# Performance work log

Measured on AMD Instinct MI355X. Metric: run time of the kernel, lower is better.

The kernel has to match this reference:

```python
import jax, jax.numpy as jnp
import numpy as np
import math

C_IN, L, D, H, DFF = 16, 1024, 128, 8, 512
B = 16
EPS = 1e-5


def layer_norm(x, g, b):
    mu = jnp.mean(x, axis=-1, keepdims=True)
    var = jnp.var(x, axis=-1, keepdims=True)
    return (x - mu) * jax.lax.rsqrt(var + EPS) * g + b


def tape_pe():
    pos = jnp.arange(L, dtype=jnp.float32)[:, None]
    div = jnp.exp(jnp.arange(0, D, 2, dtype=jnp.float32) * (-math.log(10000.0) / D))
    ang = pos * div * (D / L)  # [L, D/2]
    return jnp.stack([jnp.sin(ang), jnp.cos(ang)], axis=-1).reshape(L, D)


def setup_inputs() -> dict:
    key = jax.random.key(0)
    ks = jax.random.split(key, 16)
    d4 = 4 * D
    inp = {
        "x": jax.random.normal(ks[0], (B, C_IN, L), dtype=jnp.float32),
        "conv1_w": jax.random.normal(ks[1], (d4, 1, 1, 7), dtype=jnp.float32) * 0.2,
        "conv1_b": jnp.zeros((d4,), jnp.float32),
        "bn1_g": jnp.ones((d4,), jnp.float32),
        "bn1_b": jnp.zeros((d4,), jnp.float32),
        "conv2_w": jax.random.normal(ks[2], (D, d4, C_IN, 1), dtype=jnp.float32) * (1.0 / math.sqrt(d4 * C_IN)),
        "conv2_b": jnp.zeros((D,), jnp.float32),
        "bn2_g": jnp.ones((D,), jnp.float32),
        "bn2_b": jnp.zeros((D,), jnp.float32),
        "wq": jax.random.normal(ks[3], (D, D), dtype=jnp.float32) / math.sqrt(D),
        "wk": jax.random.normal(ks[4], (D, D), dtype=jnp.float32) / math.sqrt(D),
        "wv": jax.random.normal(ks[5], (D, D), dtype=jnp.float32) / math.sqrt(D),
        "rel_table": jax.random.normal(ks[6], (2 * L - 1, H), dtype=jnp.float32) * 0.02,
        "ln_att_g": jnp.ones((D,), jnp.float32),
        "ln_att_b": jnp.zeros((D,), jnp.float32),
        "ln1_g": jnp.ones((D,), jnp.float32),
        "ln1_b": jnp.zeros((D,), jnp.float32),
        "ln2_g": jnp.ones((D,), jnp.float32),
        "ln2_b": jnp.zeros((D,), jnp.float32),
        "ff_w1": jax.random.normal(ks[7], (DFF, D), dtype=jnp.float32) / math.sqrt(D),
        "ff_b1": jnp.zeros((DFF,), jnp.float32),
        "ff_w2": jax.random.normal(ks[8], (D, DFF), dtype=jnp.float32) / math.sqrt(DFF),
        "ff_b2": jnp.zeros((D,), jnp.float32),
    }
    return inp


def reference(x, conv1_w, conv1_b, bn1_g, bn1_b, conv2_w, conv2_b, bn2_g, bn2_b,
              wq, wk, wv, rel_table, ln_att_g, ln_att_b, ln1_g, ln1_b,
              ln2_g, ln2_b, ff_w1, ff_b1, ff_w2, ff_b2):
    dn = ("NCHW", "OIHW", "NCHW")
    h = x[:, None, :, :]  # [B,1,C_IN,L]
    h = jax.lax.conv_general_dilated(h, conv1_w, (1, 1), ((0, 0), (3, 3)), dimension_numbers=dn)
    h = h + conv1_b[None, :, None, None]
    # BatchNorm2d in eval with running_mean=0, running_var=1
    h = h * (bn1_g * (1.0 / math.sqrt(1.0 + EPS)))[None, :, None, None] + bn1_b[None, :, None, None]
    h = jax.nn.gelu(h, approximate=False)
    h = jax.lax.conv_general_dilated(h, conv2_w, (1, 1), ((0, 0), (0, 0)), dimension_numbers=dn)
    h = h + conv2_b[None, :, None, None]
    h = h * (bn2_g * (1.0 / math.sqrt(1.0 + EPS)))[None, :, None, None] + bn2_b[None, :, None, None]
    h = jax.nn.gelu(h, approximate=False)
    x_src = jnp.transpose(h[:, :, 0, :], (0, 2, 1))  # [B,L,D]

    x_pos = x_src + tape_pe()  # tAPE (dropout is identity in eval)

    dh = D // H
    scale = D ** (-0.5)  # note: full d_model, as in the source
    q = (x_pos @ wq.T).reshape(B, L, H, dh).transpose(0, 2, 1, 3)
    k = (x_pos @ wk.T).reshape(B, L, H, dh).transpose(0, 2, 1, 3)
    v = (x_pos @ wv.T).reshape(B, L, H, dh).transpose(0, 2, 1, 3)
    scores = jnp.einsum("bhqd,bhkd->bhqk", q, k) * scale
    attn = jax.nn.softmax(scores, axis=-1)
    # gathered relative-position bias added AFTER softmax (faithful to source)
    idx = jnp.arange(L)[:, None] - jnp.arange(L)[None, :] + (L - 1)  # [L,L]
    rel_bias = rel_table[idx]  # [L,L,H]
    attn = attn + jnp.transpose(rel_bias, (2, 0, 1))[None]
    out = jnp.einsum("bhqk,bhkd->bhqd", attn, v).transpose(0, 2, 1, 3).reshape(B, L, D)
    out = layer_norm(out, ln_att_g, ln_att_b)  # Attention_Rel_Scl.to_out

    att = layer_norm(x_src + out, ln1_g, ln1_b)
    ff = jax.nn.relu(att @ ff_w1.T + ff_b1) @ ff_w2.T + ff_b2
    y = layer_norm(att + ff, ln2_g, ln2_b)
    return jnp.transpose(y, (0, 2, 1))  # [B,D,L]
```

## Files before the change

### kernel.cpp

```cpp
#include <hip/hip_runtime.h>
#include <math.h>

#define BB   16
#define CIN  16
#define LL   1024
#define DD   128
#define NHH  8
#define DHH  16
#define DF   512

#define INVS 0.9999950000374998f
#define QSCALE2 0.12751743f

typedef __attribute__((ext_vector_type(4))) float f32x4;
typedef __attribute__((ext_vector_type(8))) __bf16 bf16x8;

__device__ __forceinline__ float gelu_t(float v) {
    float u = v * v;
    float a = v * fmaf(-0.07135481627f, u, -1.5957691216f);
    float e = __expf(a);
    return v * __builtin_amdgcn_rcpf(1.0f + e);
}

__device__ __forceinline__ unsigned pkbf(float a, float b) {
    union { __bf16 h[2]; unsigned u; } z;
    z.h[0] = (__bf16)a; z.h[1] = (__bf16)b;
    return z.u;
}

#define SWZ(l) ((((l) & 7) ^ (((l) >> 2) & 6)))

__global__ __launch_bounds__(256) void k_prep(
    const float* __restrict__ c2w,
    const float* __restrict__ wq, const float* __restrict__ wk,
    const float* __restrict__ wv,
    const float* __restrict__ w1f, const float* __restrict__ w2f,
    const float* __restrict__ c1w, const float* __restrict__ c1b,
    const float* __restrict__ g1,  const float* __restrict__ bb1,
    __bf16* __restrict__ w2bf,  __bf16* __restrict__ wallbf,
    __bf16* __restrict__ w1fbf, __bf16* __restrict__ w2fbf,
    float* __restrict__ peb, float* __restrict__ w1A, float* __restrict__ b1A)
{
    const int bid = blockIdx.x;
    const int t = threadIdx.x;
    if (bid < 1024) {
        int i = (bid * 256 + t) * 4;
        float4 v = *(const float4*)&c2w[i];
        union { __bf16 h[4]; float2 f2; } u;
        u.h[0] = (__bf16)v.x; u.h[1] = (__bf16)v.y;
        u.h[2] = (__bf16)v.z; u.h[3] = (__bf16)v.w;
        *(float2*)&w2bf[i] = u.f2;
    } else if (bid < 1072) {
        int e = ((bid - 1024) * 256 + t) * 4;
        int sel = e >> 14, r = e & 16383;
        const float* src = (sel == 0) ? wq : ((sel == 1) ? wk : wv);
        float sc = (sel == 0) ? QSCALE2 : 1.0f;
        float4 v = *(const float4*)&src[r];
        union { __bf16 h[4]; float2 f2; } u;
        u.h[0] = (__bf16)(v.x * sc); u.h[1] = (__bf16)(v.y * sc);
        u.h[2] = (__bf16)(v.z * sc); u.h[3] = (__bf16)(v.w * sc);
        *(float2*)&wallbf[e] = u.f2;
    } else if (bid < 1136) {
        int e = ((bid - 1072) * 256 + t) * 4;
        float4 v = *(const float4*)&w1f[e];
        union { __bf16 h[4]; float2 f2; } u;
        u.h[0] = (__bf16)v.x; u.h[1] = (__bf16)v.y;
        u.h[2] = (__bf16)v.z; u.h[3] = (__bf16)v.w;
        *(float2*)&w1fbf[e] = u.f2;
    } else if (bid < 1200) {
        int e = ((bid - 1136) * 256 + t) * 4;
        float4 v = *(const float4*)&w2f[e];
        union { __bf16 h[4]; float2 f2; } u;
        u.h[0] = (__bf16)v.x; u.h[1] = (__bf16)v.y;
        u.h[2] = (__bf16)v.z; u.h[3] = (__bf16)v.w;
        *(float2*)&w2fbf[e] = u.f2;
    } else if (bid < 1456) {
        int p = (bid - 1200) * 256 + t;
        int l = p >> 6, jj = p & 63;
        float ang = (float)l * expf(-0.14391156831212787f * (float)jj) * 0.125f;
        peb[l * 128 + jj * 2]     = sinf(ang);
        peb[l * 128 + jj * 2 + 1] = cosf(ang);
    } else {
        for (int o = t; o < DF; o += 256) {
            float A = g1[o] * INVS;
            #pragma unroll
            for (int tp = 0; tp < 7; tp++) w1A[o * 8 + tp] = c1w[o * 7 + tp] * A;
            w1A[o * 8 + 7] = 0.0f;
            b1A[o] = fmaf(c1b[o], A, bb1[o]);
        }
    }
}

__global__ __launch_bounds__(512, 4) void k_conv(
    const float* __restrict__ x,
    const float* __restrict__ w1A, const float* __restrict__ b1A,
    const __bf16* __restrict__ w2bf,
    const float* __restrict__ c2b, const float* __restrict__ g2,
    const float* __restrict__ bb2,
    float* __restrict__ xsrc)
{
    const int lt = blockIdx.x;
    const int b  = blockIdx.y;
    const int t  = threadIdx.x;
    const int l0 = lt * 32;

    __shared__ float xs[CIN][40];
    __shared__ __align__(16) __bf16 Ab[2][32 * 256];

    for (int idx = t; idx < CIN * 38; idx += 512) {
        int c = idx / 38, i = idx % 38;
        int l = l0 - 3 + i;
        xs[c][i] = (l >= 0 && l < LL) ? x[(b * CIN + c) * LL + l] : 0.0f;
    }
    __syncthreads();

    const int lane = t & 63;
    const int wv   = t >> 6;
    const int ogu  = __builtin_amdgcn_readfirstlane(wv);
    const int cp   = lane & 7;
    const int lqi  = lane >> 3;
    const int c0   = cp * 2;
    const int lq   = lqi * 4;

    float xw[2][10];
    #pragma unroll
    for (int j = 0; j < 10; j++) {
        xw[0][j] = xs[c0][lq + j];
        xw[1][j] = xs[c0 + 1][lq + j];
    }

    const int l15 = lane & 15, kg = lane >> 4;

    f32x4 acc[2];
    acc[0] = (f32x4){0.f, 0.f, 0.f, 0.f};
    acc[1] = (f32x4){0.f, 0.f, 0.f, 0.f};

    bf16x8 breg[8];

#define BLOAD(CH) do { \
    _Pragma("unroll") \
    for (int kk = 0; kk < 8; kk++) \
        breg[kk] = *(const bf16x8*)&w2bf[ \
            (size_t)(wv * 16 + l15) * 8192 + (size_t)(CH) * 256 + kk * 32 + kg * 8]; \
} while (0)

#define CONV_CHUNK(BUF, CH) do { \
    _Pragma("unroll") \
    for (int j = 0; j < 2; j++) { \
        int o = (CH) * 16 + ogu * 2 + j; \
        f32x4 wA = *(const f32x4*)&w1A[o * 8]; \
        f32x4 wB = *(const f32x4*)&w1A[o * 8 + 4]; \
        float bias = b1A[o]; \
        int kcol = (ogu * 2 + j) * 16 + c0; \
        _Pragma("unroll") \
        for (int dl = 0; dl < 4; dl++) { \
            float h2[2]; \
            _Pragma("unroll") \
            for (int ci = 0; ci < 2; ci++) { \
                float s = fmaf(xw[ci][dl], wA[0], bias); \
                s = fmaf(xw[ci][dl + 1], wA[1], s); \
                s = fmaf(xw[ci][dl + 2], wA[2], s); \
                s = fmaf(xw[ci][dl + 3], wA[3], s); \
                s = fmaf(xw[ci][dl + 4], wB[0], s); \
                s = fmaf(xw[ci][dl + 5], wB[1], s); \
                s = fmaf(xw[ci][dl + 6], wB[2], s); \
                h2[ci] = gelu_t(s); \
            } \
            int l = lq + dl; \
            *(unsigned*)&Ab[BUF][l * 256 + (kcol ^ (SWZ(l) << 3))] = pkbf(h2[0], h2[1]); \
        } \
    } \
} while (0)

#define MFMA_CHUNK(BUF) do { \
    _Pragma("unroll") \
    for (int kk = 0; kk < 8; kk++) { \
        int kb = kk * 32 + kg * 8; \
        _Pragma("unroll") \
        for (int mf = 0; mf < 2; mf++) { \
            int r = mf * 16 + l15; \
            bf16x8 af = *(const bf16x8*)&Ab[BUF][r * 256 + (kb ^ (SWZ(r) << 3))]; \
            acc[mf] = __builtin_amdgcn_mfma_f32_16x16x32_bf16(af, breg[kk], acc[mf], 0, 0, 0); \
        } \
    } \
} while (0)

    BLOAD(0);
    CONV_CHUNK(0, 0);
    __syncthreads();

    for (int ic = 0; ic < 30; ic += 2) {
        MFMA_CHUNK(0);
        BLOAD(ic + 1);
        CONV_CHUNK(1, ic + 1);
        __syncthreads();

        MFMA_CHUNK(1);
        BLOAD(ic + 2);
        CONV_CHUNK(0, ic + 2);
        __syncthreads();
    }
    MFMA_CHUNK(0);
    BLOAD(31);
    CONV_CHUNK(1, 31);
    __syncthreads();
    MFMA_CHUNK(1);

    {
        int d = wv * 16 + l15;
        float A2 = g2[d] * INVS;
        float B2 = fmaf(c2b[d], A2, bb2[d]);
        #pragma unroll
        for (int mf = 0; mf < 2; mf++) {
            #pragma unroll
            for (int r = 0; r < 4; r++) {
                int l = l0 + mf * 16 + kg * 4 + r;
                xsrc[((size_t)b * LL + l) * DD + d] = gelu_t(fmaf(acc[mf][r], A2, B2));
            }
        }
    }
#undef BLOAD
#undef CONV_CHUNK
#undef MFMA_CHUNK
}

__global__ __launch_bounds__(384) void k_qkv(
    const float* __restrict__ xsrc, const float* __restrict__ peb,
    const __bf16* __restrict__ wallbf,
    __bf16* __restrict__ qo, __bf16* __restrict__ ko, __bf16* __restrict__ vo)
{
    const int lt = blockIdx.x, b = blockIdx.y;
    const int t = threadIdx.x;
    const int l0 = lt * 64;

    __shared__ __align__(16) __bf16 Xp[64 * 128];

    for (int e = t; e < 2048; e += 384) {
        int l = e >> 5, d0 = (e & 31) * 4;
        float4 xv = *(const float4*)&xsrc[((size_t)b * LL + l0 + l) * DD + d0];
        float4 pv = *(const float4*)&peb[(size_t)(l0 + l) * DD + d0];
        union { __bf16 h[4]; float2 f2; } u;
        u.h[0] = (__bf16)(xv.x + pv.x); u.h[1] = (__bf16)(xv.y + pv.y);
        u.h[2] = (__bf16)(xv.z + pv.z); u.h[3] = (__bf16)(xv.w + pv.w);
        *(float2*)&Xp[l * 128 + (d0 ^ (SWZ(l) << 3))] = u.f2;
    }
    __syncthreads();

    const int w = t >> 6, lane = t & 63;
    const int l15 = lane & 15, kg = lane >> 4;
    const int wsel = w >> 1, hb = w & 1;

    bf16x8 breg[16];
    #pragma unroll
    for (int nf = 0; nf < 4; nf++)
        #pragma unroll
        for (int kk = 0; kk < 4; kk++)
            breg[nf * 4 + kk] = *(const bf16x8*)&wallbf[
                (size_t)wsel * 16384 + (size_t)(hb * 64 + nf * 16 + l15) * 128 + kk * 32 + kg * 8];

    f32x4 acc[4][4];
    #pragma unroll
    for (int mf = 0; mf < 4; mf++)
        #pragma unroll
        for (int nf = 0; nf < 4; nf++) acc[mf][nf] = (f32x4){0.f, 0.f, 0.f, 0.f};

    #pragma unroll
    for (int kk = 0; kk < 4; kk++) {
        int kb = kk * 32 + kg * 8;
        bf16x8 af[4];
        #pragma unroll
        for (int mf = 0; mf < 4; mf++) {
            int r = mf * 16 + l15;
            af[mf] = *(const bf16x8*)&Xp[r * 128 + (kb ^ (SWZ(r) << 3))];
        }
        #pragma unroll
        for (int mf = 0; mf < 4; mf++)
            #pragma unroll
            for (int nf = 0; nf < 4; nf++)
                acc[mf][nf] = __builtin_amdgcn_mfma_f32_16x16x32_bf16(
                    af[mf], breg[nf * 4 + kk], acc[mf][nf], 0, 0, 0);
    }

    __bf16* op = (wsel == 0) ? qo : ((wsel == 1) ? ko : vo);
    #pragma unroll
    for (int mf = 0; mf < 4; mf++) {
        #pragma unroll
        for (int nf = 0; nf < 4; nf++) {
            int h = hb * 4 + nf;
            #pragma unroll
            for (int r = 0; r < 4; r++) {
                int l = l0 + mf * 16 + kg * 4 + r;
                op[(((size_t)b * NHH + h) * LL + l) * DHH + l15] = (__bf16)acc[mf][nf][r];
            }
        }
    }
}

__global__ __launch_bounds__(256) void k_attn(
    const __bf16* __restrict__ q, const __bf16* __restrict__ k,
    const __bf16* __restrict__ v, const float* __restrict__ rel,
    float* __restrict__ out)
{
    const int bh = blockIdx.x;
    const int qt = blockIdx.y;
    const int h  = bh & 7;
    const int t  = threadIdx.x;
    const int w  = t >> 6, lane = t & 63;
    const int g  = lane >> 4, qi = lane & 15;
    const int xq = (qi & 7) << 3;
    const int qbase = qt * 128 + w * 32;

    __shared__ __align__(16) __bf16 lds[16384];
    __bf16* Vl = lds;
    __bf16* Pw = lds + 4096 + w * 2048;
    __bf16* R0 = lds + 12288;
    __bf16* R1 = lds + 14336;

    for (int i = t; i < 2048; i += 256) {
        R0[i] = (__bf16)((i <= 2046) ? rel[(size_t)(2046 - i) * NHH + h] : 0.0f);
        R1[i] = (__bf16)((i <= 2045) ? rel[(size_t)(2045 - i) * NHH + h] : 0.0f);
    }

    bf16x8 qf[2];
    {
        union { unsigned u[4]; bf16x8 v8; } uz;
        uz.u[0] = uz.u[1] = uz.u[2] = uz.u[3] = 0u;
        #pragma unroll
        for (int n = 0; n < 2; n++) {
            qf[n] = uz.v8;
            if (g < 2)
                qf[n] = *(const bf16x8*)&q[((size_t)bh * LL + qbase + n * 16 + qi) * DHH + g * 8];
        }
    }

    f32x4 accp[2], accb[2];
    #pragma unroll
    for (int n = 0; n < 2; n++) {
        accp[n] = (f32x4){0.f, 0.f, 0.f, 0.f};
        accb[n] = (f32x4){0.f, 0.f, 0.f, 0.f};
    }
    float mrun[2] = {-INFINITY, -INFINITY};
    float lrun[2] = {0.f, 0.f};

    const f32x4 zero4 = (f32x4){0.f, 0.f, 0.f, 0.f};

#define PROC_N(Sn, n) do { \
    float mx = Sn[0][0]; \
    _Pragma("unroll") \
    for (int f = 0; f < 8; f++) { \
        _Pragma("unroll") \
        for (int r = 0; r < 4; r++) if (f || r) mx = fmaxf(mx, Sn[f][r]); } \
    mx = fmaxf(mx, __shfl_xor(mx, 16, 64)); \
    mx = fmaxf(mx, __shfl_xor(mx, 32, 64)); \
    float mnew = fmaxf(mrun[n], mx); \
    float sf = __builtin_amdgcn_exp2f(mrun[n] - mnew); \
    mrun[n] = mnew; \
    lrun[n] *= sf; \
    accp[n][0] *= sf; accp[n][1] *= sf; accp[n][2] *= sf; accp[n][3] *= sf; \
    float ls = 0.f; \
    _Pragma("unroll") \
    for (int f = 0; f < 8; f++) { \
        float p0 = __builtin_amdgcn_exp2f(Sn[f][0] - mnew); \
        float p1 = __builtin_amdgcn_exp2f(Sn[f][1] - mnew); \
        float p2 = __builtin_amdgcn_exp2f(Sn[f][2] - mnew); \
        float p3 = __builtin_amdgcn_exp2f(Sn[f][3] - mnew); \
        ls += (p0 + p1) + (p2 + p3); \
        unsigned* pp = (unsigned*)(Pw + (qi * 128 + ((f * 16 + g * 4) ^ xq))); \
        pp[0] = pkbf(p0, p1); pp[1] = pkbf(p2, p3); \
    } \
    ls += __shfl_xor(ls, 16, 64); ls += __shfl_xor(ls, 32, 64); \
    lrun[n] += ls; \
    int qoff = 1023 - (qbase + (n) * 16 + qi) + k0; \
    _Pragma("unroll") \
    for (int c = 0; c < 4; c++) { \
        bf16x8 vf = *(const bf16x8*)&Vbuf[qi * 128 + ((c * 32 + g * 8) ^ xq)]; \
        bf16x8 pf = *(const bf16x8*)&Pw[qi * 128 + ((c * 32 + g * 8) ^ xq)]; \
        int idx = qoff + c * 32 + 8 * g; \
        const unsigned* tb = (const unsigned*)((idx & 1) ? R1 : R0); \
        unsigned s_ = (unsigned)idx >> 1; \
        union { unsigned u[4]; bf16x8 v8; } bu; \
        bu.u[0] = tb[s_]; bu.u[1] = tb[s_ + 1]; \
        bu.u[2] = tb[s_ + 2]; bu.u[3] = tb[s_ + 3]; \
        accp[n] = __builtin_amdgcn_mfma_f32_16x16x32_bf16(vf, pf, accp[n], 0, 0, 0); \
        accb[n] = __builtin_amdgcn_mfma_f32_16x16x32_bf16(vf, bu.v8, accb[n], 0, 0, 0); \
    } \
} while (0)

    for (int kt = 0; kt < 8; kt++) {
        const int k0 = kt * 128;
        {
            int kr = t >> 1, d0 = (t & 1) * 8;
            bf16x8 b8 = *(const bf16x8*)&v[((size_t)bh * LL + k0 + kr) * DHH + d0];
            __bf16* dst = Vl + (kt & 1) * 2048;
            #pragma unroll
            for (int i = 0; i < 8; i++) {
                int d = d0 + i;
                dst[d * 128 + (kr ^ ((d & 7) << 3))] = b8[i];
            }
        }
        __syncthreads();
        const __bf16* Vbuf = Vl + (kt & 1) * 2048;

        f32x4 S0[8], S1[8];
        #pragma unroll
        for (int f = 0; f < 8; f++) {
            bf16x8 kf = *(const bf16x8*)&k[((size_t)bh * LL + k0 + f * 16 + qi) * DHH + (g & 1) * 8];
            S0[f] = __builtin_amdgcn_mfma_f32_16x16x32_bf16(kf, qf[0], zero4, 0, 0, 0);
            S1[f] = __builtin_amdgcn_mfma_f32_16x16x32_bf16(kf, qf[1], zero4, 0, 0, 0);
        }

        PROC_N(S0, 0);
        PROC_N(S1, 1);
    }
#undef PROC_N

    #pragma unroll
    for (int n = 0; n < 2; n++) {
        float inv = 1.0f / lrun[n];
        float4 o;
        o.x = accp[n][0] * inv + accb[n][0];
        o.y = accp[n][1] * inv + accb[n][1];
        o.z = accp[n][2] * inv + accb[n][2];
        o.w = accp[n][3] * inv + accb[n][3];
        *(float4*)&out[((size_t)bh * LL + qbase + n * 16 + qi) * DHH + g * 4] = o;
    }
}

__global__ __launch_bounds__(256) void k_ln(
    const float* __restrict__ ao,  const float* __restrict__ xsrc,
    const float* __restrict__ lag, const float* __restrict__ lab,
    const float* __restrict__ l1g, const float* __restrict__ l1b,
    float* __restrict__ att)
{
    const int lt = blockIdx.x, b = blockIdx.y;
    const int t = threadIdx.x;
    const int l0 = lt * 64;
    __shared__ float tile[64][132];

    #pragma unroll
    for (int u = 0; u < 4; u++) {
        int cid = u * 256 + t;
        int hh = cid >> 7, rem = cid & 127;
        int l = rem >> 1, dh0 = (rem & 1) * 8;
        const float* src = &ao[(((size_t)b * NHH + hh) * LL + l0 + l) * DHH + dh0];
        float4 a0 = *(const float4*)src;
        float4 a1 = *(const float4*)(src + 4);
        *(float4*)&tile[l][hh * 16 + dh0]     = a0;
        *(float4*)&tile[l][hh * 16 + dh0 + 4] = a1;
    }
    __syncthreads();

    const int wid = t >> 6, lane = t & 63;
    float2 ga  = *(const float2*)&lag[lane * 2];
    float2 ba  = *(const float2*)&lab[lane * 2];
    float2 g1v = *(const float2*)&l1g[lane * 2];
    float2 b1v = *(const float2*)&l1b[lane * 2];

    for (int rr = 0; rr < 16; rr++) {
        int r = wid * 16 + rr;
        float2 vv = *(const float2*)&tile[r][lane * 2];
        float s = vv.x + vv.y, s2 = vv.x * vv.x + vv.y * vv.y;
        #pragma unroll
        for (int m = 1; m < 64; m <<= 1) { s += __shfl_xor(s, m, 64); s2 += __shfl_xor(s2, m, 64); }
        float mu = s * (1.f / 128.f);
        float var = s2 * (1.f / 128.f) - mu * mu;
        float rs = rsqrtf(var + 1e-5f);
        float o0 = (vv.x - mu) * rs * ga.x + ba.x;
        float o1 = (vv.y - mu) * rs * ga.y + ba.y;
        float2 xv = *(const float2*)&xsrc[((size_t)b * LL + l0 + r) * DD + lane * 2];
        float t0 = xv.x + o0, t1 = xv.y + o1;
        s = t0 + t1; s2 = t0 * t0 + t1 * t1;
        #pragma unroll
        for (int m = 1; m < 64; m <<= 1) { s += __shfl_xor(s, m, 64); s2 += __shfl_xor(s2, m, 64); }
        mu = s * (1.f / 128.f);
        var = s2 * (1.f / 128.f) - mu * mu;
        rs = rsqrtf(var + 1e-5f);
        float a0 = (t0 - mu) * rs * g1v.x + b1v.x;
        float a1 = (t1 - mu) * rs * g1v.y + b1v.y;
        float2 o = {a0, a1};
        *(float2*)&att[((size_t)b * LL + l0 + r) * DD + lane * 2] = o;
    }
}

__global__ __launch_bounds__(512) void k_ff1(
    const float* __restrict__ att, const __bf16* __restrict__ w1fbf,
    const float* __restrict__ b1f, __bf16* __restrict__ ff1b)
{
    const int lt = blockIdx.x, b = blockIdx.y;
    const int t = threadIdx.x;
    const int l0 = lt * 64;

    __shared__ __align__(16) __bf16 Ax[64 * 128];

    #pragma unroll
    for (int it = 0; it < 4; it++) {
        int e = it * 512 + t;
        int l = e >> 5, d0 = (e & 31) * 4;
        float4 xv = *(const float4*)&att[((size_t)b * LL + l0 + l) * DD + d0];
        union { __bf16 h[4]; float2 f2; } u;
        u.h[0] = (__bf16)xv.x; u.h[1] = (__bf16)xv.y;
        u.h[2] = (__bf16)xv.z; u.h[3] = (__bf16)xv.w;
        *(float2*)&Ax[l * 128 + (d0 ^ (SWZ(l) << 3))] = u.f2;
    }
    __syncthreads();

    const int w = t >> 6, lane = t & 63;
    const int l15 = lane & 15, kg = lane >> 4;

    bf16x8 breg[16];
    #pragma unroll
    for (int nf = 0; nf < 4; nf++)
        #pragma unroll
        for (int kk = 0; kk < 4; kk++)
            breg[nf * 4 + kk] = *(const bf16x8*)&w1fbf[
                (size_t)(w * 64 + nf * 16 + l15) * 128 + kk * 32 + kg * 8];

    f32x4 acc[4][4];
    #pragma unroll
    for (int mf = 0; mf < 4; mf++)
        #pragma unroll
        for (int nf = 0; nf < 4; nf++) acc[mf][nf] = (f32x4){0.f, 0.f, 0.f, 0.f};

    #pragma unroll
    for (int kk = 0; kk < 4; kk++) {
        int kb = kk * 32 + kg * 8;
        bf16x8 af[4];
        #pragma unroll
        for (int mf = 0; mf < 4; mf++) {
            int r = mf * 16 + l15;
            af[mf] = *(const bf16x8*)&Ax[r * 128 + (kb ^ (SWZ(r) << 3))];
        }
        #pragma unroll
        for (int mf = 0; mf < 4; mf++)
            #pragma unroll
            for (int nf = 0; nf < 4; nf++)
                acc[mf][nf] = __builtin_amdgcn_mfma_f32_16x16x32_bf16(
                    af[mf], breg[nf * 4 + kk], acc[mf][nf], 0, 0, 0);
    }

    #pragma unroll
    for (int nf = 0; nf < 4; nf++) {
        int n = w * 64 + nf * 16 + l15;
        float bias = b1f[n];
        #pragma unroll
        for (int mf = 0; mf < 4; mf++) {
            #pragma unroll
            for (int r = 0; r < 4; r++) {
                int l = l0 + mf * 16 + kg * 4 + r;
                float vv = fmaxf(acc[mf][nf][r] + bias, 0.0f);
                ff1b[((size_t)b * LL + l) * DF + n] = (__bf16)vv;
            }
        }
    }
}

__global__ __launch_bounds__(512) void k_ff2(
    const __bf16* __restrict__ ff1b, const __bf16* __restrict__ w2fbf,
    const float* __restrict__ b2f, const float* __restrict__ att,
    const float* __restrict__ l2g, const float* __restrict__ l2b,
    float* __restrict__ y)
{
    const int lt = blockIdx.x, b = blockIdx.y;
    const int t = threadIdx.x;
    const int l0 = lt * 64;

    __shared__ __align__(16) __bf16 Ax[64 * 512];
    float* yl = (float*)Ax;

    #pragma unroll
    for (int it = 0; it < 8; it++) {
        int g8 = it * 512 + t;
        int l = g8 >> 6, c8 = g8 & 63;
        bf16x8 v8 = *(const bf16x8*)&ff1b[((size_t)b * LL + l0 + l) * DF + c8 * 8];
        *(bf16x8*)&Ax[l * 512 + ((c8 * 8) ^ (SWZ(l) << 3))] = v8;
    }
    __syncthreads();

    const int w = t >> 6, lane = t & 63;
    const int l15 = lane & 15, kg = lane >> 4;
    const int d = w * 16 + l15;

    bf16x8 breg[16];
    #pragma unroll
    for (int kk = 0; kk < 16; kk++)
        breg[kk] = *(const bf16x8*)&w2fbf[(size_t)d * DF + kk * 32 + kg * 8];

    f32x4 acc[4];
    #pragma unroll
    for (int mf = 0; mf < 4; mf++) acc[mf] = (f32x4){0.f, 0.f, 0.f, 0.f};

    #pragma unroll
    for (int kk = 0; kk < 16; kk++) {
        int kb = kk * 32 + kg * 8;
        #pragma unroll
        for (int mf = 0; mf < 4; mf++) {
            int r = mf * 16 + l15;
            bf16x8 af = *(const bf16x8*)&Ax[r * 512 + (kb ^ (SWZ(r) << 3))];
            acc[mf] = __builtin_amdgcn_mfma_f32_16x16x32_bf16(af, breg[kk], acc[mf], 0, 0, 0);
        }
    }
    __syncthreads();

    {
        float bias = b2f[d];
        #pragma unroll
        for (int mf = 0; mf < 4; mf++) {
            #pragma unroll
            for (int r = 0; r < 4; r++) {
                int l = mf * 16 + kg * 4 + r;
                float res = att[((size_t)b * LL + l0 + l) * DD + d];
                yl[l * 132 + d] = acc[mf][r] + bias + res;
            }
        }
    }
    __syncthreads();

    const int wid = t >> 6;
    float2 gv = *(const float2*)&l2g[lane * 2];
    float2 bv = *(const float2*)&l2b[lane * 2];
    for (int rr = 0; rr < 8; rr++) {
        int r = wid * 8 + rr;
        float2 vv = *(const float2*)&yl[r * 132 + lane * 2];
        float s = vv.x + vv.y, s2 = vv.x * vv.x + vv.y * vv.y;
        #pragma unroll
        for (int m = 1; m < 64; m <<= 1) { s += __shfl_xor(s, m, 64); s2 += __shfl_xor(s2, m, 64); }
        float mu = s * (1.f / 128.f);
        float var = s2 * (1.f / 128.f) - mu * mu;
        float rs = rsqrtf(var + 1e-5f);
        float o0 = (vv.x - mu) * rs * gv.x + bv.x;
        float o1 = (vv.y - mu) * rs * gv.y + bv.y;
        yl[r * 132 + lane * 2]     = o0;
        yl[r * 132 + lane * 2 + 1] = o1;
    }
    __syncthreads();

    {
        int dd = t >> 2, lh = (t & 3) * 16;
        #pragma unroll
        for (int i0 = 0; i0 < 16; i0 += 4) {
            float4 o = { yl[(lh + i0 + 0) * 132 + dd], yl[(lh + i0 + 1) * 132 + dd],
                         yl[(lh + i0 + 2) * 132 + dd], yl[(lh + i0 + 3) * 132 + dd] };
            *(float4*)&y[(size_t)b * DD * LL + (size_t)dd * LL + l0 + lh + i0] = o;
        }
    }
}

extern "C" void kernel_launch(void* const* d_in, const int* in_sizes, int n_in,
                              void* d_out, int out_size, void* d_ws, size_t ws_size,
                              hipStream_t stream)
{
    const float* x   = (const float*)d_in[0];
    const float* c1w = (const float*)d_in[1];
    const float* c1b = (const float*)d_in[2];
    const float* g1  = (const float*)d_in[3];
    const float* bb1 = (const float*)d_in[4];
    const float* c2w = (const float*)d_in[5];
    const float* c2b = (const float*)d_in[6];
    const float* g2  = (const float*)d_in[7];
    const float* bb2 = (const float*)d_in[8];
    const float* wq  = (const float*)d_in[9];
    const float* wk  = (const float*)d_in[10];
    const float* wv  = (const float*)d_in[11];
    const float* rel = (const float*)d_in[12];
    const float* lag = (const float*)d_in[13];
    const float* lab = (const float*)d_in[14];
    const float* l1g = (const float*)d_in[15];
    const float* l1b = (const float*)d_in[16];
    const float* l2g = (const float*)d_in[17];
    const float* l2b = (const float*)d_in[18];
    const float* w1f = (const float*)d_in[19];
    const float* b1f = (const float*)d_in[20];
    const float* w2f = (const float*)d_in[21];
    const float* b2f = (const float*)d_in[22];

    char* W = (char*)d_ws;
    const size_t MB = 1ull << 20;
    float*  xsrc   = (float*)(W);
    float*  abuf   = (float*)(W + 8 * MB);
    float*  attb   = (float*)(W + 16 * MB);
    __bf16* qbuf   = (__bf16*)(W + 24 * MB);
    __bf16* kbuf   = (__bf16*)(W + 28 * MB);
    __bf16* vbuf   = (__bf16*)(W + 32 * MB);
    __bf16* ff1b   = (__bf16*)(W + 36 * MB);
    __bf16* w2bf   = (__bf16*)(W + 52 * MB);
    __bf16* wallbf = (__bf16*)(W + 54 * MB);
    __bf16* w1fbf  = (__bf16*)(W + 54 * MB + 128 * 1024);
    __bf16* w2fbf  = (__bf16*)(W + 54 * MB + 256 * 1024);
    float*  peb    = (float*)(W + 54 * MB + 384 * 1024);
    float*  w1A    = (float*)(W + 54 * MB + 896 * 1024);
    float*  b1A    = (float*)(W + 54 * MB + 912 * 1024);

    k_prep<<<dim3(1457), dim3(256), 0, stream>>>(
        c2w, wq, wk, wv, w1f, w2f, c1w, c1b, g1, bb1,
        w2bf, wallbf, w1fbf, w2fbf, peb, w1A, b1A);
    k_conv<<<dim3(32, 16), dim3(512), 0, stream>>>(x, w1A, b1A, w2bf, c2b, g2, bb2, xsrc);
    k_qkv<<<dim3(16, 16), dim3(384), 0, stream>>>(xsrc, peb, wallbf, qbuf, kbuf, vbuf);
    k_attn<<<dim3(128, 8), dim3(256), 0, stream>>>(qbuf, kbuf, vbuf, rel, abuf);
    k_ln<<<dim3(16, 16), dim3(256), 0, stream>>>(abuf, xsrc, lag, lab, l1g, l1b, attb);
    k_ff1<<<dim3(16, 16), dim3(512), 0, stream>>>(attb, w1fbf, b1f, ff1b);
    k_ff2<<<dim3(16, 16), dim3(512), 0, stream>>>(ff1b, w2fbf, b2f, attb, l2g, l2b, (float*)d_out);
}
```

Measured before the change: 239.1 us.

## Split conv K-reduction across two blocks with a separate finalize kernel

The fused conv kernel's K dimension (4D*C_IN channels) is split in half across a new grid z dimension, so it launches twice as many blocks, each processing 16 chunks instead of 32. Partial sums go to a workspace buffer, and a new elementwise kernel adds the two partials and applies the BN2 affine and GELU. The aim is better occupancy of the GPU's compute units, since the original 512-block grid was likely too small. The cost is an extra launch plus roughly 16 MB of partial-sum writes and reads. The partial buffer overlaps abuf, which is safe only because abuf is written later.

```diff
diff --git a/kernel.cpp b/kernel.cpp
--- a/kernel.cpp
+++ b/kernel.cpp
@@ -95,12 +95,11 @@
     const float* __restrict__ x,
     const float* __restrict__ w1A, const float* __restrict__ b1A,
     const __bf16* __restrict__ w2bf,
-    const float* __restrict__ c2b, const float* __restrict__ g2,
-    const float* __restrict__ bb2,
-    float* __restrict__ xsrc)
+    float* __restrict__ part)
 {
     const int lt = blockIdx.x;
     const int b  = blockIdx.y;
+    const int kh = blockIdx.z;
     const int t  = threadIdx.x;
     const int l0 = lt * 32;
 
@@ -130,6 +129,8 @@
     }
 
     const int l15 = lane & 15, kg = lane >> 4;
+    const int kbase = kh * 4096;
+    const int obase = kh * 256;
 
     f32x4 acc[2];
     acc[0] = (f32x4){0.f, 0.f, 0.f, 0.f};
@@ -141,13 +142,13 @@
     _Pragma("unroll") \
     for (int kk = 0; kk < 8; kk++) \
         breg[kk] = *(const bf16x8*)&w2bf[ \
-            (size_t)(wv * 16 + l15) * 8192 + (size_t)(CH) * 256 + kk * 32 + kg * 8]; \
+            (size_t)(wv * 16 + l15) * 8192 + (size_t)(kbase + (CH) * 256) + kk * 32 + kg * 8]; \
 } while (0)
 
 #define CONV_CHUNK(BUF, CH) do { \
     _Pragma("unroll") \
     for (int j = 0; j < 2; j++) { \
-        int o = (CH) * 16 + ogu * 2 + j; \
+        int o = obase + (CH) * 16 + ogu * 2 + j; \
         f32x4 wA = *(const f32x4*)&w1A[o * 8]; \
         f32x4 wB = *(const f32x4*)&w1A[o * 8 + 4]; \
         float bias = b1A[o]; \
@@ -189,7 +190,7 @@
     CONV_CHUNK(0, 0);
     __syncthreads();
 
-    for (int ic = 0; ic < 30; ic += 2) {
+    for (int ic = 0; ic < 14; ic += 2) {
         MFMA_CHUNK(0);
         BLOAD(ic + 1);
         CONV_CHUNK(1, ic + 1);
@@ -201,27 +202,52 @@
         __syncthreads();
     }
     MFMA_CHUNK(0);
-    BLOAD(31);
-    CONV_CHUNK(1, 31);
+    BLOAD(15);
+    CONV_CHUNK(1, 15);
     __syncthreads();
     MFMA_CHUNK(1);
 
     {
         int d = wv * 16 + l15;
-        float A2 = g2[d] * INVS;
-        float B2 = fmaf(c2b[d], A2, bb2[d]);
+        float* pp = part + (size_t)kh * (BB * LL * DD);
         #pragma unroll
         for (int mf = 0; mf < 2; mf++) {
             #pragma unroll
             for (int r = 0; r < 4; r++) {
                 int l = l0 + mf * 16 + kg * 4 + r;
-                xsrc[((size_t)b * LL + l) * DD + d] = gelu_t(fmaf(acc[mf][r], A2, B2));
+                pp[((size_t)b * LL + l) * DD + d] = acc[mf][r];
             }
         }
     }
 #undef BLOAD
 #undef CONV_CHUNK
 #undef MFMA_CHUNK
+}
+
+__global__ __launch_bounds__(256) void k_convfin(
+    const float* __restrict__ part, const float* __restrict__ c2b,
+    const float* __restrict__ g2,   const float* __restrict__ bb2,
+    float* __restrict__ xsrc)
+{
+    size_t i = ((size_t)blockIdx.x * 256 + threadIdx.x) * 4;
+    int d0 = (int)(i & (DD - 1));
+    float4 p0 = *(const float4*)&part[i];
+    float4 p1 = *(const float4*)&part[(size_t)BB * LL * DD + i];
+    float4 gv = *(const float4*)&g2[d0];
+    float4 cb = *(const float4*)&c2b[d0];
+    float4 bv = *(const float4*)&bb2[d0];
+    float pv[4] = {p0.x + p1.x, p0.y + p1.y, p0.z + p1.z, p0.w + p1.w};
+    float gg[4] = {gv.x, gv.y, gv.z, gv.w};
+    float cc[4] = {cb.x, cb.y, cb.z, cb.w};
+    float bb_[4] = {bv.x, bv.y, bv.z, bv.w};
+    float r[4];
+    #pragma unroll
+    for (int j = 0; j < 4; j++) {
+        float A = gg[j] * INVS;
+        r[j] = gelu_t(fmaf(pv[j], A, fmaf(cc[j], A, bb_[j])));
+    }
+    float4 o = {r[0], r[1], r[2], r[3]};
+    *(float4*)&xsrc[i] = o;
 }
 
 __global__ __launch_bounds__(384) void k_qkv(
@@ -676,6 +702,7 @@
     char* W = (char*)d_ws;
     const size_t MB = 1ull << 20;
     float*  xsrc   = (float*)(W);
+    float*  part   = (float*)(W + 8 * MB);
     float*  abuf   = (float*)(W + 8 * MB);
     float*  attb   = (float*)(W + 16 * MB);
     __bf16* qbuf   = (__bf16*)(W + 24 * MB);
@@ -693,7 +720,8 @@
     k_prep<<<dim3(1457), dim3(256), 0, stream>>>(
         c2w, wq, wk, wv, w1f, w2f, c1w, c1b, g1, bb1,
         w2bf, wallbf, w1fbf, w2fbf, peb, w1A, b1A);
-    k_conv<<<dim3(32, 16), dim3(512), 0, stream>>>(x, w1A, b1A, w2bf, c2b, g2, bb2, xsrc);
+    k_conv<<<dim3(32, 16, 2), dim3(512), 0, stream>>>(x, w1A, b1A, w2bf, part);
+    k_convfin<<<dim3(2048), dim3(256), 0, stream>>>(part, c2b, g2, bb2, xsrc);
     k_qkv<<<dim3(16, 16), dim3(384), 0, stream>>>(xsrc, peb, wallbf, qbuf, kbuf, vbuf);
     k_attn<<<dim3(128, 8), dim3(256), 0, stream>>>(qbuf, kbuf, vbuf, rel, abuf);
     k_ln<<<dim3(16, 16), dim3(256), 0, stream>>>(abuf, xsrc, lag, lab, l1g, l1b, attb);
```

New measurement: 246.0 us. +2.9%, slower.
